# Kernel optimization log

Measured on AMD Instinct MI355X. Metric: run time of the kernel, lower is better.

## Reference

```python
import jax, jax.numpy as jnp
import numpy as np

B, R, C, H, W = 4, 2, 19, 256, 512


def setup_inputs() -> dict:
    key = jax.random.key(0)
    k1, k2, k3 = jax.random.split(key, 3)
    return {
        "ref_pred": jax.random.normal(k1, (B, R, C, H, W), dtype=jnp.float32),
        # motion vectors in quarter-pel units (divided by 4 inside forward);
        # scale so displacements span a few pixels
        "ref_mv": jax.random.normal(k2, (B, R, 2, H, W), dtype=jnp.float32) * 8.0,
        "ref_weight": jax.random.uniform(k3, (B, R, 1, H, W), dtype=jnp.float32),
    }


def _warp(img, mv):
    """Bilinear backward warp (grid_sample, zeros padding).
    img: [N, C, H, W], mv: [N, 2, H, W] pixel displacements (x, y)."""
    N, Ch, Hh, Ww = img.shape
    ys, xs = jnp.meshgrid(jnp.arange(Hh, dtype=mv.dtype),
                          jnp.arange(Ww, dtype=mv.dtype), indexing="ij")
    gx = xs + mv[:, 0]  # [N, H, W] sample x-coordinate
    gy = ys + mv[:, 1]  # [N, H, W] sample y-coordinate
    x0 = jnp.floor(gx); y0 = jnp.floor(gy)
    x1 = x0 + 1.0;      y1 = y0 + 1.0
    wx1 = gx - x0; wx0 = 1.0 - wx1
    wy1 = gy - y0; wy0 = 1.0 - wy1

    img_flat = img.reshape(N, Ch, Hh * Ww)

    def samp(iy, ix):
        valid = ((ix >= 0) & (ix <= Ww - 1) & (iy >= 0) & (iy <= Hh - 1))
        iyc = jnp.clip(iy, 0, Hh - 1).astype(jnp.int32)
        ixc = jnp.clip(ix, 0, Ww - 1).astype(jnp.int32)
        lin = (iyc * Ww + ixc).reshape(N, 1, Hh * Ww)
        vals = jnp.take_along_axis(
            img_flat, jnp.broadcast_to(lin, (N, Ch, Hh * Ww)), axis=2
        ).reshape(N, Ch, Hh, Ww)
        return vals * valid.astype(img.dtype)[:, None]

    out = (samp(y0, x0) * (wy0 * wx0)[:, None]
           + samp(y0, x1) * (wy0 * wx1)[:, None]
           + samp(y1, x0) * (wy1 * wx0)[:, None]
           + samp(y1, x1) * (wy1 * wx1)[:, None])
    return out


def reference(ref_pred, ref_mv, ref_weight):
    Bb, Rr = ref_pred.shape[:2]
    pred = ref_pred.reshape(Bb * Rr, *ref_pred.shape[2:])   # [B*R, C, H, W]
    mv = ref_mv.reshape(Bb * Rr, *ref_mv.shape[2:]) / 4.0    # quarter-pel -> pixel
    # eval mode, eval_noise_sigma=0 -> no noise added
    warped = _warp(pred, mv)                                  # [B*R, C, H, W]
    w = ref_weight.reshape(Bb * Rr, *ref_weight.shape[2:])   # [B*R, 1, H, W]
    warped = warped * w
    return warped.reshape(Bb, Rr, *warped.shape[1:]).sum(axis=1)  # [B, C, H, W]
```

## Files before the change

kernel.cpp:

```cpp
#include <hip/hip_runtime.h>

constexpr int B = 4, R = 2, C = 19, H = 256, W = 512;
constexpr int HW = H * W;

constexpr int BX = 64, BY = 16;
constexpr int NBX = W / BX;
constexpr int NBY = H / BY;
constexpr int NSPAT = B * NBX * NBY;
constexpr int NCHUNK = 4;

constexpr int TW = 88;
constexpr int TH = 37;
constexpr int TILE_N = TW * TH;
constexpr int TILE_V4 = TILE_N / 4;

#define GLD_LDS16(gsrc, ldst)                                                  \
    __builtin_amdgcn_global_load_lds(                                          \
        (const __attribute__((address_space(1))) void*)(gsrc),                 \
        (__attribute__((address_space(3))) void*)(ldst), 16, 0, 0)

__global__ __launch_bounds__(256, 4) void mc_warp_kernel(
    const float* __restrict__ pred,
    const float* __restrict__ mv,
    const float* __restrict__ wgt,
    float* __restrict__ out)
{
    __shared__ float tiles[2][TILE_N];

    int t = threadIdx.x;
    int xcd  = blockIdx.x & 7;
    int slot = blockIdx.x >> 3;
    int vblk = xcd * (NSPAT / 8) + slot;
    int bx   = vblk & (NBX - 1);
    int by   = (vblk >> 3) & (NBY - 1);
    int b    = vblk >> 7;
    int x0 = bx * BX, y0 = by * BY;
    int lane = t & 63, wv = t >> 6;
    int x  = x0 + lane;
    int yb = y0 + wv * 4;

    int rowbase = min(max(y0 - 10, 0), H - TH);
    int colbase = min(max(x0 - 12, 0), W - TW);

    const float* pl0 = pred + (size_t)(b * R + 0) * C * HW;
    const float* pl1 = pred + (size_t)(b * R + 1) * C * HW;
    const float* st0 = pl0 + (size_t)rowbase * W + colbase;
    const float* st1 = pl1 + (size_t)rowbase * W + colbase;

    int cbeg = (C * blockIdx.y) / NCHUNK;
    int cend = (C * (blockIdx.y + 1)) / NCHUNK;

    {
        const float* s0 = st0 + (size_t)cbeg * HW;
        const float* s1 = st1 + (size_t)cbeg * HW;
        #pragma unroll
        for (int i = 0; i < 4; ++i) {
            int idx = t + i * 256;
            if (idx < TILE_V4) {
                int row = idx / 22;
                int off = idx * 4 + row * (W - TW);
                GLD_LDS16(s0 + off, &tiles[0][idx * 4]);
                GLD_LDS16(s1 + off, &tiles[1][idx * 4]);
            }
        }
    }

    int   off0[R][4], off1[R][4];
    int   offL0[R][4], offL1[R][4], offG0[R][4], offG1[R][4];
    float wq[R][4][4];
    int flag = 0;

    #pragma unroll
    for (int r = 0; r < R; ++r) {
        const float* mvx = mv + (size_t)((b * R + r) * 2) * HW;
        const float* mvy = mvx + HW;
        const float* wp  = wgt + (size_t)(b * R + r) * HW;
        #pragma unroll
        for (int p = 0; p < 4; ++p) {
            int yy = yb + p;
            size_t ro = (size_t)yy * W + x;
            float mx = mvx[ro], my = mvy[ro], wr = wp[ro];

            float gx = (float)x  + mx * 0.25f;
            float gy = (float)yy + my * 0.25f;
            float fx0 = floorf(gx), fy0 = floorf(gy);
            float wx1 = gx - fx0, wx0 = 1.0f - wx1;
            float wy1 = gy - fy0, wy0 = 1.0f - wy1;
            int ix0 = (int)fx0, iy0 = (int)fy0;
            int ix1 = ix0 + 1,  iy1 = iy0 + 1;

            int base = min(max(ix0, 0), W - 2);
            float wA = (ix0 == base)     ? wx0 : ((ix1 == base)     ? wx1 : 0.0f);
            float wB = (ix1 == base + 1) ? wx1 : ((ix0 == base + 1) ? wx0 : 0.0f);
            float wy0v = ((iy0 >= 0) && (iy0 < H)) ? wy0 * wr : 0.0f;
            float wy1v = ((iy1 >= 0) && (iy1 < H)) ? wy1 * wr : 0.0f;
            int cy0 = min(max(iy0, 0), H - 1);
            int cy1 = min(max(iy1, 0), H - 1);

            int l0 = base - colbase;
            int r0 = cy0 - rowbase, r1 = cy1 - rowbase;
            bool anyx = (wA != 0.0f) || (wB != 0.0f);
            bool anyy = (wy0v != 0.0f) || (wy1v != 0.0f);
            bool cb  = (l0 < 0 || l0 > TW - 2) && anyx && anyy;
            bool rb0 = (r0 < 0 || r0 > TH - 1) && (wy0v != 0.0f) && anyx;
            bool rb1 = (r1 < 0 || r1 > TH - 1) && (wy1v != 0.0f) && anyx;
            flag |= (int)(cb || rb0 || rb1);
            l0 = min(max(l0, 0), TW - 2);
            r0 = min(max(r0, 0), TH - 1);
            r1 = min(max(r1, 0), TH - 1);

            offL0[r][p] = r0 * TW + l0;
            offL1[r][p] = r1 * TW + l0;
            offG0[r][p] = cy0 * W + base;
            offG1[r][p] = cy1 * W + base;
            wq[r][p][0] = wy0v * wA;
            wq[r][p][1] = wy0v * wB;
            wq[r][p][2] = wy1v * wA;
            wq[r][p][3] = wy1v * wB;
        }
    }

    int fbB = __syncthreads_or(flag);
    #pragma unroll
    for (int r = 0; r < R; ++r)
        #pragma unroll
        for (int p = 0; p < 4; ++p) {
            off0[r][p] = fbB ? offG0[r][p] : offL0[r][p];
            off1[r][p] = fbB ? offG1[r][p] : offL1[r][p];
        }

    float* ob = out + (size_t)b * C * HW + (size_t)yb * W + x;

    for (int c = cbeg; c < cend; ++c) {
        if (c > cbeg) {
            __syncthreads();
            if (!fbB) {
                const float* s0 = st0 + (size_t)c * HW;
                const float* s1 = st1 + (size_t)c * HW;
                #pragma unroll
                for (int i = 0; i < 4; ++i) {
                    int idx = t + i * 256;
                    if (idx < TILE_V4) {
                        int row = idx / 22;
                        int off = idx * 4 + row * (W - TW);
                        GLD_LDS16(s0 + off, &tiles[0][idx * 4]);
                        GLD_LDS16(s1 + off, &tiles[1][idx * 4]);
                    }
                }
            }
        }
        __syncthreads();

        float res[4];
        if (!fbB) {
            const float* tb0 = &tiles[0][0];
            const float* tb1 = &tiles[1][0];
            #pragma unroll
            for (int p = 0; p < 4; ++p) {
                float a00 = tb0[off0[0][p]], a01 = tb0[off0[0][p] + 1];
                float a10 = tb0[off1[0][p]], a11 = tb0[off1[0][p] + 1];
                float b00 = tb1[off0[1][p]], b01 = tb1[off0[1][p] + 1];
                float b10 = tb1[off1[1][p]], b11 = tb1[off1[1][p] + 1];
                res[p] = wq[0][p][0] * a00 + wq[0][p][1] * a01
                       + wq[0][p][2] * a10 + wq[0][p][3] * a11
                       + wq[1][p][0] * b00 + wq[1][p][1] * b01
                       + wq[1][p][2] * b10 + wq[1][p][3] * b11;
            }
        } else {
            const float* pc0 = pl0 + (size_t)c * HW;
            const float* pc1 = pl1 + (size_t)c * HW;
            #pragma unroll
            for (int p = 0; p < 4; ++p) {
                float a00 = pc0[off0[0][p]], a01 = pc0[off0[0][p] + 1];
                float a10 = pc0[off1[0][p]], a11 = pc0[off1[0][p] + 1];
                float b00 = pc1[off0[1][p]], b01 = pc1[off0[1][p] + 1];
                float b10 = pc1[off1[1][p]], b11 = pc1[off1[1][p] + 1];
                res[p] = wq[0][p][0] * a00 + wq[0][p][1] * a01
                       + wq[0][p][2] * a10 + wq[0][p][3] * a11
                       + wq[1][p][0] * b00 + wq[1][p][1] * b01
                       + wq[1][p][2] * b10 + wq[1][p][3] * b11;
            }
        }
        float* oc = ob + (size_t)c * HW;
        #pragma unroll
        for (int p = 0; p < 4; ++p)
            oc[(size_t)p * W] = res[p];
    }
}

extern "C" void kernel_launch(void* const* d_in, const int* in_sizes, int n_in,
                              void* d_out, int out_size, void* d_ws, size_t ws_size,
                              hipStream_t stream) {
    const float* pred = (const float*)d_in[0];
    const float* mv   = (const float*)d_in[1];
    const float* wgt  = (const float*)d_in[2];
    float* out = (float*)d_out;

    dim3 grid(NSPAT, NCHUNK);
    mc_warp_kernel<<<grid, dim3(256), 0, stream>>>(pred, mv, wgt, out);
}
```

Before: 148.4 us.

## Assign one channel per block instead of looping over channel chunks

The grid goes from 4 channel chunks to 19, one per channel, so each block loads a single channel tile pair and writes one output channel. The per-block channel loop and its intermediate barriers are removed. This is meant to raise parallelism and let many blocks overlap memory latency. In exchange, the motion-vector and weight loads and the bilinear coefficient setup are now repeated for every channel instead of being shared across about five channels.

```diff
diff --git a/kernel.cpp b/kernel.cpp
--- a/kernel.cpp
+++ b/kernel.cpp
@@ -7,7 +7,6 @@
 constexpr int NBX = W / BX;
 constexpr int NBY = H / BY;
 constexpr int NSPAT = B * NBX * NBY;
-constexpr int NCHUNK = 4;
 
 constexpr int TW = 88;
 constexpr int TH = 37;
@@ -34,6 +33,7 @@
     int bx   = vblk & (NBX - 1);
     int by   = (vblk >> 3) & (NBY - 1);
     int b    = vblk >> 7;
+    int c    = blockIdx.y;
     int x0 = bx * BX, y0 = by * BY;
     int lane = t & 63, wv = t >> 6;
     int x  = x0 + lane;
@@ -44,15 +44,12 @@
 
     const float* pl0 = pred + (size_t)(b * R + 0) * C * HW;
     const float* pl1 = pred + (size_t)(b * R + 1) * C * HW;
-    const float* st0 = pl0 + (size_t)rowbase * W + colbase;
-    const float* st1 = pl1 + (size_t)rowbase * W + colbase;
-
-    int cbeg = (C * blockIdx.y) / NCHUNK;
-    int cend = (C * (blockIdx.y + 1)) / NCHUNK;
+    const float* pc0 = pl0 + (size_t)c * HW;
+    const float* pc1 = pl1 + (size_t)c * HW;
 
     {
-        const float* s0 = st0 + (size_t)cbeg * HW;
-        const float* s1 = st1 + (size_t)cbeg * HW;
+        const float* s0 = pc0 + (size_t)rowbase * W + colbase;
+        const float* s1 = pc1 + (size_t)rowbase * W + colbase;
         #pragma unroll
         for (int i = 0; i < 4; ++i) {
             int idx = t + i * 256;
@@ -129,63 +126,41 @@
             off1[r][p] = fbB ? offG1[r][p] : offL1[r][p];
         }
 
-    float* ob = out + (size_t)b * C * HW + (size_t)yb * W + x;
+    __syncthreads();
 
-    for (int c = cbeg; c < cend; ++c) {
-        if (c > cbeg) {
-            __syncthreads();
-            if (!fbB) {
-                const float* s0 = st0 + (size_t)c * HW;
-                const float* s1 = st1 + (size_t)c * HW;
-                #pragma unroll
-                for (int i = 0; i < 4; ++i) {
-                    int idx = t + i * 256;
-                    if (idx < TILE_V4) {
-                        int row = idx / 22;
-                        int off = idx * 4 + row * (W - TW);
-                        GLD_LDS16(s0 + off, &tiles[0][idx * 4]);
-                        GLD_LDS16(s1 + off, &tiles[1][idx * 4]);
-                    }
-                }
-            }
+    float res[4];
+    if (!fbB) {
+        const float* tb0 = &tiles[0][0];
+        const float* tb1 = &tiles[1][0];
+        #pragma unroll
+        for (int p = 0; p < 4; ++p) {
+            float a00 = tb0[off0[0][p]], a01 = tb0[off0[0][p] + 1];
+            float a10 = tb0[off1[0][p]], a11 = tb0[off1[0][p] + 1];
+            float b00 = tb1[off0[1][p]], b01 = tb1[off0[1][p] + 1];
+            float b10 = tb1[off1[1][p]], b11 = tb1[off1[1][p] + 1];
+            res[p] = wq[0][p][0] * a00 + wq[0][p][1] * a01
+                   + wq[0][p][2] * a10 + wq[0][p][3] * a11
+                   + wq[1][p][0] * b00 + wq[1][p][1] * b01
+                   + wq[1][p][2] * b10 + wq[1][p][3] * b11;
         }
-        __syncthreads();
+    } else {
+        #pragma unroll
+        for (int p = 0; p < 4; ++p) {
+            float a00 = pc0[off0[0][p]], a01 = pc0[off0[0][p] + 1];
+            float a10 = pc0[off1[0][p]], a11 = pc0[off1[0][p] + 1];
+            float b00 = pc1[off0[1][p]], b01 = pc1[off0[1][p] + 1];
+            float b10 = pc1[off1[1][p]], b11 = pc1[off1[1][p] + 1];
+            res[p] = wq[0][p][0] * a00 + wq[0][p][1] * a01
+                   + wq[0][p][2] * a10 + wq[0][p][3] * a11
+                   + wq[1][p][0] * b00 + wq[1][p][1] * b01
+                   + wq[1][p][2] * b10 + wq[1][p][3] * b11;
+        }
+    }
 
-        float res[4];
-        if (!fbB) {
-            const float* tb0 = &tiles[0][0];
-            const float* tb1 = &tiles[1][0];
-            #pragma unroll
-            for (int p = 0; p < 4; ++p) {
-                float a00 = tb0[off0[0][p]], a01 = tb0[off0[0][p] + 1];
-                float a10 = tb0[off1[0][p]], a11 = tb0[off1[0][p] + 1];
-                float b00 = tb1[off0[1][p]], b01 = tb1[off0[1][p] + 1];
-                float b10 = tb1[off1[1][p]], b11 = tb1[off1[1][p] + 1];
-                res[p] = wq[0][p][0] * a00 + wq[0][p][1] * a01
-                       + wq[0][p][2] * a10 + wq[0][p][3] * a11
-                       + wq[1][p][0] * b00 + wq[1][p][1] * b01
-                       + wq[1][p][2] * b10 + wq[1][p][3] * b11;
-            }
-        } else {
-            const float* pc0 = pl0 + (size_t)c * HW;
-            const float* pc1 = pl1 + (size_t)c * HW;
-            #pragma unroll
-            for (int p = 0; p < 4; ++p) {
-                float a00 = pc0[off0[0][p]], a01 = pc0[off0[0][p] + 1];
-                float a10 = pc0[off1[0][p]], a11 = pc0[off1[0][p] + 1];
-                float b00 = pc1[off0[1][p]], b01 = pc1[off0[1][p] + 1];
-                float b10 = pc1[off1[1][p]], b11 = pc1[off1[1][p] + 1];
-                res[p] = wq[0][p][0] * a00 + wq[0][p][1] * a01
-                       + wq[0][p][2] * a10 + wq[0][p][3] * a11
-                       + wq[1][p][0] * b00 + wq[1][p][1] * b01
-                       + wq[1][p][2] * b10 + wq[1][p][3] * b11;
-            }
-        }
-        float* oc = ob + (size_t)c * HW;
-        #pragma unroll
-        for (int p = 0; p < 4; ++p)
-            oc[(size_t)p * W] = res[p];
-    }
+    float* oc = out + (size_t)b * C * HW + (size_t)c * HW + (size_t)yb * W + x;
+    #pragma unroll
+    for (int p = 0; p < 4; ++p)
+        oc[(size_t)p * W] = res[p];
 }
 
 extern "C" void kernel_launch(void* const* d_in, const int* in_sizes, int n_in,
@@ -196,6 +171,6 @@
     const float* wgt  = (const float*)d_in[2];
     float* out = (float*)d_out;
 
-    dim3 grid(NSPAT, NCHUNK);
+    dim3 grid(NSPAT, C);
     mc_warp_kernel<<<grid, dim3(256), 0, stream>>>(pred, mv, wgt, out);
 }
```

Result: slower. 161.3 us (+8.7%).
